# Kernel tuning notes

Hardware: AMD Instinct MI355X
Metric: run time of the kernel (lower is better)

Reference implementation:

```python
import jax, jax.numpy as jnp
import numpy as np
import math

B, N, D = 64, 512, 1024
SHELL_DIM, RFF_DIM, ORDER = 64, 32, 4
CHARGE_COUPLING, SHELL_COUPLING = 1.0, 0.5
DIST_COUPLING, DIST_SCALE = 0.3, 10.0
COMBINED_DIM = 64


def setup_inputs() -> dict:
    key = jax.random.key(0)
    ks = jax.random.split(key, 12)
    s = 0.02
    inp = {
        "x": jax.random.normal(ks[0], (B, N, D), dtype=jnp.float32),
        "W_charge": jax.random.normal(ks[1], (1, D), dtype=jnp.float32) * s,
        "b_charge": jnp.zeros((1,), dtype=jnp.float32),
        "W_shell": jax.random.normal(ks[2], (SHELL_DIM, D), dtype=jnp.float32) * s,
        "b_shell": jnp.zeros((SHELL_DIM,), dtype=jnp.float32),
        # RFF params (learnable=True in source): omega ~ N(0,1)*sqrt(coupling), bias ~ U(0, 2pi)
        "omega": jax.random.normal(ks[3], (RFF_DIM, SHELL_DIM), dtype=jnp.float32) * math.sqrt(SHELL_COUPLING),
        "rff_bias": jax.random.uniform(ks[4], (RFF_DIM,), dtype=jnp.float32) * (2.0 * math.pi),
        "W_combine": jax.random.normal(ks[5], (COMBINED_DIM, (ORDER + 1) * 2 * RFF_DIM), dtype=jnp.float32) * s,
        "W_v": jax.random.normal(ks[6], (D, D), dtype=jnp.float32) * s,
        "b_v": jnp.zeros((D,), dtype=jnp.float32),
        "W_out": jax.random.normal(ks[7], (D, D), dtype=jnp.float32) * s,
        "b_out": jnp.zeros((D,), dtype=jnp.float32),
        "log_temp": jnp.zeros((), dtype=jnp.float32),
    }
    return inp


def _forward(x, W_charge, b_charge, W_shell, b_shell, omega, rff_bias,
             W_combine, W_v, b_v, W_out, b_out, log_temp):
    b, n, d = x.shape
    # charge: (B,N) in [-1,1]
    q = jnp.tanh(x @ W_charge.T + b_charge)[..., 0]
    # polynomial charge features: sqrt(|(-k)^n/n!| + 1e-10) * q^n, n=0..ORDER
    coeffs = jnp.asarray([(-CHARGE_COUPLING) ** m / math.factorial(m) for m in range(ORDER + 1)], dtype=x.dtype)
    mags = jnp.sqrt(jnp.abs(coeffs) + 1e-10)  # (5,)
    phi_c = mags * q[..., None] ** jnp.arange(ORDER + 1)  # (B,N,5)
    # shell: normalized linear projection
    shell = x @ W_shell.T + b_shell
    shell = shell / jnp.maximum(jnp.linalg.norm(shell, axis=-1, keepdims=True), 1e-12)
    # random Fourier features
    proj = shell @ omega.T + rff_bias  # (B,N,RFF)
    rff_scale = math.sqrt(2.0 / (2 * RFF_DIM)) * math.sqrt(math.exp(-SHELL_COUPLING))
    phi_s = jnp.concatenate([jnp.cos(proj), jnp.sin(proj)], axis=-1) * rff_scale  # (B,N,64)
    # tensor product -> combine projection (no bias)
    tp = (phi_c[..., :, None] * phi_s[..., None, :]).reshape(b, n, -1)  # (B,N,5*64)
    phi = tp @ W_combine.T  # (B,N,64)
    # Toeplitz distance weighting exp(-coupling*|i-j|/scale)
    idx = jnp.arange(n)
    T = jnp.exp(-DIST_COUPLING * jnp.abs(idx[:, None] - idx[None, :]).astype(x.dtype) / DIST_SCALE)
    temp = jax.nn.softplus(log_temp) + 0.1
    logits = jnp.einsum('bnd,bmd->bnm', phi, phi) * T / temp
    # causal mask (allow j <= i)
    causal = idx[:, None] >= idx[None, :]
    logits = jnp.where(causal, logits, -jnp.inf)
    attn = jax.nn.softmax(logits, axis=-1)
    V = x @ W_v.T + b_v
    out = jnp.einsum('bnm,bmd->bnd', attn, V)
    return out @ W_out.T + b_out


def reference(x, W_charge, b_charge, W_shell, b_shell, omega, rff_bias,
              W_combine, W_v, b_v, W_out, b_out, log_temp):
    return _forward(x, W_charge, b_charge, W_shell, b_shell, omega, rff_bias,
                    W_combine, W_v, b_v, W_out, b_out, log_temp)
```

## Files before the change

kernel.cpp:

```cpp
#include <hip/hip_runtime.h>
#include <hip/hip_bf16.h>
#include <math.h>


using u16 = unsigned short;
typedef short short8 __attribute__((ext_vector_type(8)));
typedef float f32x4 __attribute__((ext_vector_type(4)));

__device__ __forceinline__ u16 f2bf(float f) {
  unsigned u = __float_as_uint(f);
  return (u16)((u + 0x7fffu + ((u >> 16) & 1u)) >> 16);
}

__global__ __launch_bounds__(256) void convert_x_kernel(const float* __restrict__ in,
                                                        u16* __restrict__ out, int n4) {
  int idx = blockIdx.x * 256 + threadIdx.x;
  int stride = gridDim.x * 256;
  for (int i = idx; i < n4; i += stride) {
    float4 v = reinterpret_cast<const float4*>(in)[i];
    ushort4 o;
    o.x = f2bf(v.x); o.y = f2bf(v.y); o.z = f2bf(v.z); o.w = f2bf(v.w);
    reinterpret_cast<ushort4*>(out)[i] = o;
  }
}

__global__ __launch_bounds__(256) void prep_weights_kernel(
    const float* __restrict__ Wv, const float* __restrict__ Wo,
    const float* __restrict__ Wsh, const float* __restrict__ Wch,
    const float* __restrict__ Wcb,
    u16* __restrict__ wvb, u16* __restrict__ wob,
    u16* __restrict__ wcat, u16* __restrict__ wcbb) {
  int i = blockIdx.x * 256 + threadIdx.x;
  if (i < 1048576) { wvb[i] = f2bf(Wv[i]); return; }
  i -= 1048576;
  if (i < 1048576) { wob[i] = f2bf(Wo[i]); return; }
  i -= 1048576;
  if (i < 131072) {
    int row = i >> 10, e = i & 1023;
    float v = (row < 64) ? Wsh[i] : ((row == 64) ? Wch[e] : 0.0f);
    wcat[i] = f2bf(v);
    return;
  }
  i -= 131072;
  if (i < 40960) {
    int row = i / 320;
    wcbb[i] = f2bf(row < 64 ? Wcb[i] : 0.0f);
  }
}

template<int OUT_MODE>
__global__ __launch_bounds__(256) void gemm_bt(
    const u16* __restrict__ A, const u16* __restrict__ Bt,
    const float* __restrict__ bias, void* __restrict__ Cv,
    int M, int N, int K, int lda, int ldb, int ldc,
    long long sA, long long sB, long long sC) {
  (void)M; (void)N;
  __shared__ u16 lA[128 * 32];
  __shared__ u16 lB[128 * 32];
  const int t = threadIdx.x;
  const int lane = t & 63;
  const int w = t >> 6;
  const u16* Ag = A + (size_t)blockIdx.z * sA;
  const u16* Bg = Bt + (size_t)blockIdx.z * sB;
  const int m0 = blockIdx.y * 128;
  const int n0 = blockIdx.x * 128;
  const int wm = (w >> 1) * 64;
  const int wn = (w & 1) * 64;
  const int rl = lane & 15;
  const int kl = (lane >> 4) * 8;
  const int r0 = t >> 2;
  const int c0 = (t & 3) * 8;

  f32x4 acc[4][4] = {};

  for (int k0 = 0; k0 < K; k0 += 32) {
    #pragma unroll
    for (int ch = 0; ch < 2; ++ch) {
      const int row = ch * 64 + r0;
      short8 va = *reinterpret_cast<const short8*>(Ag + (size_t)(m0 + row) * lda + k0 + c0);
      short8 vb = *reinterpret_cast<const short8*>(Bg + (size_t)(n0 + row) * ldb + k0 + c0);
      *reinterpret_cast<short8*>(&lA[row * 32 + c0]) = va;
      *reinterpret_cast<short8*>(&lB[row * 32 + c0]) = vb;
    }
    __syncthreads();
    short8 af[4], bfr[4];
    #pragma unroll
    for (int mi = 0; mi < 4; ++mi)
      af[mi] = *reinterpret_cast<const short8*>(&lA[(wm + mi * 16 + rl) * 32 + kl]);
    #pragma unroll
    for (int ni = 0; ni < 4; ++ni)
      bfr[ni] = *reinterpret_cast<const short8*>(&lB[(wn + ni * 16 + rl) * 32 + kl]);
    #pragma unroll
    for (int mi = 0; mi < 4; ++mi) {
      #pragma unroll
      for (int ni = 0; ni < 4; ++ni)
        acc[mi][ni] = __builtin_amdgcn_mfma_f32_16x16x32_bf16(af[mi], bfr[ni], acc[mi][ni], 0, 0, 0);
    }
    __syncthreads();
  }

  const int cm = (lane >> 4) * 4;
  #pragma unroll
  for (int mi = 0; mi < 4; ++mi) {
    #pragma unroll
    for (int ni = 0; ni < 4; ++ni) {
      const int gm = m0 + wm + mi * 16 + cm;
      const int gn = n0 + wn + ni * 16 + rl;
      const float bsv = bias ? bias[gn] : 0.0f;
      if (OUT_MODE == 0) {
        float* C = (float*)Cv + (size_t)blockIdx.z * sC;
        #pragma unroll
        for (int r = 0; r < 4; ++r)
          C[(size_t)(gm + r) * ldc + gn] = acc[mi][ni][r] + bsv;
      } else if (OUT_MODE == 1) {
        u16* C = (u16*)Cv + (size_t)blockIdx.z * sC;
        #pragma unroll
        for (int r = 0; r < 4; ++r)
          C[(size_t)(gm + r) * ldc + gn] = f2bf(acc[mi][ni][r] + bsv);
      } else {
        u16* C = (u16*)Cv + (size_t)blockIdx.z * sC;
        ushort4 pk;
        pk.x = f2bf(acc[mi][ni][0] + bsv);
        pk.y = f2bf(acc[mi][ni][1] + bsv);
        pk.z = f2bf(acc[mi][ni][2] + bsv);
        pk.w = f2bf(acc[mi][ni][3] + bsv);
        *reinterpret_cast<ushort4*>(&C[(size_t)gn * ldc + gm]) = pk;
      }
    }
  }
}

__global__ __launch_bounds__(256) void features_kernel(
    const float* __restrict__ SC, const float* __restrict__ b_shell,
    const float* __restrict__ b_charge, const float* __restrict__ omega,
    const float* __restrict__ rff_bias, u16* __restrict__ tp) {
  __shared__ __align__(16) float sm[4][64];
  const int lane = threadIdx.x & 63;
  const int w = threadIdx.x >> 6;
  const int row = blockIdx.x * 4 + w;
  const float* sc = SC + (size_t)row * 128;
  float s = sc[lane] + b_shell[lane];
  float ss = s * s;
  #pragma unroll
  for (int off = 32; off > 0; off >>= 1) ss += __shfl_xor(ss, off);
  float shell = s / fmaxf(sqrtf(ss), 1e-12f);
  sm[w][lane] = shell;
  const float q = tanhf(sc[64] + b_charge[0]);
  __syncthreads();
  const int r = lane & 31;
  float p = rff_bias[r];
  const float4* om = reinterpret_cast<const float4*>(omega + r * 64);
  const float4* sv = reinterpret_cast<const float4*>(sm[w]);
  #pragma unroll
  for (int d = 0; d < 16; ++d) {
    float4 o4 = om[d], s4 = sv[d];
    p += o4.x * s4.x + o4.y * s4.y + o4.z * s4.z + o4.w * s4.w;
  }
  const float RFFS = 0.13767388f;
  float phis = (lane < 32) ? cosf(p) * RFFS : sinf(p) * RFFS;
  float q2 = q * q;
  float pc[5];
  pc[0] = 1.0f;
  pc[1] = q;
  pc[2] = 0.70710678f * q2;
  pc[3] = 0.40824829f * q2 * q;
  pc[4] = 0.20412415f * q2 * q2;
  u16* o = tp + (size_t)row * 320 + lane;
  #pragma unroll
  for (int m = 0; m < 5; ++m) o[m * 64] = f2bf(pc[m] * phis);
}

__global__ __launch_bounds__(256) void softmax_kernel(
    const float* __restrict__ logits, const float* __restrict__ log_temp,
    u16* __restrict__ attn) {
  __shared__ float rb[8];
  const int rowid = blockIdx.x;
  const int i = rowid & 511;
  const float* L = logits + (size_t)rowid * 512;
  u16* Ar = attn + (size_t)rowid * 512;
  const int t = threadIdx.x, lane = t & 63, w = t >> 6;
  const float invt = 1.0f / (log1pf(expf(log_temp[0])) + 0.1f);
  const int j0 = t, j1 = t + 256;
  float z0 = (j0 <= i) ? L[j0] * expf(-0.03f * (float)(i - j0)) * invt : -INFINITY;
  float z1 = (j1 <= i) ? L[j1] * expf(-0.03f * (float)(i - j1)) * invt : -INFINITY;
  float m = fmaxf(z0, z1);
  #pragma unroll
  for (int off = 32; off > 0; off >>= 1) m = fmaxf(m, __shfl_xor(m, off));
  if (lane == 0) rb[w] = m;
  __syncthreads();
  m = fmaxf(fmaxf(rb[0], rb[1]), fmaxf(rb[2], rb[3]));
  float e0 = expf(z0 - m);
  float e1 = expf(z1 - m);
  float sum = e0 + e1;
  #pragma unroll
  for (int off = 32; off > 0; off >>= 1) sum += __shfl_xor(sum, off);
  if (lane == 0) rb[4 + w] = sum;
  __syncthreads();
  const float inv = 1.0f / (rb[4] + rb[5] + rb[6] + rb[7]);
  Ar[j0] = f2bf(e0 * inv);
  Ar[j1] = f2bf(e1 * inv);
}

extern "C" void kernel_launch(void* const* d_in, const int* in_sizes, int n_in,
                              void* d_out, int out_size, void* d_ws, size_t ws_size,
                              hipStream_t stream) {
  (void)in_sizes; (void)n_in; (void)out_size; (void)ws_size;
  const float* x     = (const float*)d_in[0];
  const float* Wch   = (const float*)d_in[1];
  const float* bch   = (const float*)d_in[2];
  const float* Wsh   = (const float*)d_in[3];
  const float* bsh   = (const float*)d_in[4];
  const float* omega = (const float*)d_in[5];
  const float* rffb  = (const float*)d_in[6];
  const float* Wcb   = (const float*)d_in[7];
  const float* Wv    = (const float*)d_in[8];
  const float* bv    = (const float*)d_in[9];
  const float* Wo    = (const float*)d_in[10];
  const float* bo    = (const float*)d_in[11];
  const float* lt    = (const float*)d_in[12];
  float* out = (float*)d_out;
  char* ws = (char*)d_ws;

  u16*   xb   = (u16*)(ws + 0);
  u16*   vt   = (u16*)(ws + 67108864);
  float* sc   = (float*)(ws + 67108864);
  u16*   attn = (u16*)(ws + 134217728);
  u16*   tp   = (u16*)(ws + 134217728);
  u16*   phi  = (u16*)(ws + 167772160);
  u16*   wvb  = (u16*)(ws + 176160768);
  u16*   wob  = (u16*)(ws + 178257920);
  u16*   wcat = (u16*)(ws + 180355072);
  u16*   wcbb = (u16*)(ws + 180617216);
  float* logits = out;
  u16*   out2 = xb;

  convert_x_kernel<<<8192, 256, 0, stream>>>(x, xb, 33554432 / 4);
  prep_weights_kernel<<<8864, 256, 0, stream>>>(Wv, Wo, Wsh, Wch, Wcb, wvb, wob, wcat, wcbb);
  gemm_bt<0><<<dim3(1, 256, 1), 256, 0, stream>>>(xb, wcat, nullptr, sc,
      32768, 128, 1024, 1024, 1024, 128, 0, 0, 0);
  features_kernel<<<8192, 256, 0, stream>>>(sc, bsh, bch, omega, rffb, tp);
  gemm_bt<1><<<dim3(1, 256, 1), 256, 0, stream>>>(tp, wcbb, nullptr, phi,
      32768, 128, 320, 320, 320, 128, 0, 0, 0);
  gemm_bt<0><<<dim3(4, 4, 64), 256, 0, stream>>>(phi, phi, nullptr, logits,
      512, 512, 64, 128, 128, 512, 65536, 65536, 262144);
  softmax_kernel<<<32768, 256, 0, stream>>>(logits, lt, attn);
  gemm_bt<2><<<dim3(8, 256, 1), 256, 0, stream>>>(xb, wvb, bv, vt,
      32768, 1024, 1024, 1024, 1024, 32768, 0, 0, 0);
  gemm_bt<1><<<dim3(8, 4, 64), 256, 0, stream>>>(attn, vt, nullptr, out2,
      512, 1024, 512, 512, 32768, 1024, 262144, 512, 524288);
  gemm_bt<0><<<dim3(8, 256, 1), 256, 0, stream>>>(out2, wob, bo, out,
      32768, 1024, 1024, 1024, 1024, 1024, 0, 0, 0);
}
```

Measured before the change: 718.9 us.

## Load GEMM tiles directly into LDS and swizzle blocks across XCDs

Replaces the register round-trip for staging A and B tiles with direct global-to-LDS loads, each wave filling a contiguous 32-row slab. Adds a block-index remap that groups neighbouring tiles onto the same XCD to improve L2 reuse. This cuts VGPR use and instruction count in the load phase. It relies on the barrier waiting for outstanding async loads, and the remap changes tile locality.

```diff
diff --git a/kernel.cpp b/kernel.cpp
--- a/kernel.cpp
+++ b/kernel.cpp
@@ -10,6 +10,13 @@
 __device__ __forceinline__ u16 f2bf(float f) {
   unsigned u = __float_as_uint(f);
   return (u16)((u + 0x7fffu + ((u >> 16) & 1u)) >> 16);
+}
+
+__device__ __forceinline__ void gload16(const u16* g, u16* l) {
+  __builtin_amdgcn_global_load_lds(
+      (const __attribute__((address_space(1))) unsigned int*)(g),
+      (__attribute__((address_space(3))) unsigned int*)(l),
+      16, 0, 0);
 }
 
 __global__ __launch_bounds__(256) void convert_x_kernel(const float* __restrict__ in,
@@ -62,26 +69,36 @@
   const int w = t >> 6;
   const u16* Ag = A + (size_t)blockIdx.z * sA;
   const u16* Bg = Bt + (size_t)blockIdx.z * sB;
-  const int m0 = blockIdx.y * 128;
-  const int n0 = blockIdx.x * 128;
+
+  int gx = gridDim.x, gy = gridDim.y;
+  int bid = blockIdx.y * gx + blockIdx.x;
+  int nwg = gx * gy;
+  if ((nwg & 7) == 0) {
+    int cpx = nwg >> 3;
+    bid = (bid & 7) * cpx + (bid >> 3);
+  }
+  const int m0 = (bid / gx) * 128;
+  const int n0 = (bid % gx) * 128;
+
   const int wm = (w >> 1) * 64;
   const int wn = (w & 1) * 64;
   const int rl = lane & 15;
   const int kl = (lane >> 4) * 8;
-  const int r0 = t >> 2;
-  const int c0 = (t & 3) * 8;
+
+  const int rs = w * 32 + (lane >> 2);
+  const int cs = (lane & 3) * 8;
+  u16* ldsA = &lA[w * 1024];
+  u16* ldsB = &lB[w * 1024];
 
   f32x4 acc[4][4] = {};
 
   for (int k0 = 0; k0 < K; k0 += 32) {
-    #pragma unroll
-    for (int ch = 0; ch < 2; ++ch) {
-      const int row = ch * 64 + r0;
-      short8 va = *reinterpret_cast<const short8*>(Ag + (size_t)(m0 + row) * lda + k0 + c0);
-      short8 vb = *reinterpret_cast<const short8*>(Bg + (size_t)(n0 + row) * ldb + k0 + c0);
-      *reinterpret_cast<short8*>(&lA[row * 32 + c0]) = va;
-      *reinterpret_cast<short8*>(&lB[row * 32 + c0]) = vb;
-    }
+    const u16* ga = Ag + (size_t)(m0 + rs) * lda + k0 + cs;
+    const u16* gb = Bg + (size_t)(n0 + rs) * ldb + k0 + cs;
+    gload16(ga,                      ldsA);
+    gload16(ga + (size_t)16 * lda,   ldsA + 512);
+    gload16(gb,                      ldsB);
+    gload16(gb + (size_t)16 * ldb,   ldsB + 512);
     __syncthreads();
     short8 af[4], bfr[4];
     #pragma unroll
```

New measurement: 684.9 us. 1.05x faster.
